# Performance work log

Hardware: AMD Instinct MI355X
Metric: run time of the kernel (lower is better)

The kernel has to match this reference:

```python
import jax, jax.numpy as jnp
import numpy as np

N_NODES = 100000
N_EDGES = 3200000
NODE_DIM = 128
MRI_DIM, COG_DIM, CLIN_DIM, GEN_DIM = 256, 64, 32, 512
N_GRAPHS = 256
N_CLASSES = 3
HID = 16


def setup_inputs() -> dict:
    key = jax.random.key(0)
    ks = jax.random.split(key, 20)
    inp = {
        "x": jax.random.normal(ks[0], (N_NODES, NODE_DIM), jnp.float32),
        "edge_index": jax.random.randint(ks[1], (2, N_EDGES), 0, N_NODES, jnp.int64),
        "batch": jnp.sort(jax.random.randint(ks[2], (N_NODES,), 0, N_GRAPHS, jnp.int64)),
        "mri": jax.random.normal(ks[3], (N_GRAPHS, MRI_DIM), jnp.float32),
        "cog": jax.random.normal(ks[4], (N_GRAPHS, COG_DIM), jnp.float32),
        "clin": jax.random.normal(ks[5], (N_GRAPHS, CLIN_DIM), jnp.float32),
        "genetic": jax.random.normal(ks[6], (N_GRAPHS, GEN_DIM), jnp.float32),
        # GCNConv weight/bias
        "gcn_W": jax.random.normal(ks[7], (NODE_DIM, HID), jnp.float32) / np.sqrt(NODE_DIM),
        "gcn_b": jnp.zeros((HID,), jnp.float32),
        # modality FCs (each -> 4)
        "mri_W": jax.random.normal(ks[8], (MRI_DIM, 4), jnp.float32) / np.sqrt(MRI_DIM),
        "mri_b": jnp.zeros((4,), jnp.float32),
        "cog_W": jax.random.normal(ks[9], (COG_DIM, 4), jnp.float32) / np.sqrt(COG_DIM),
        "cog_b": jnp.zeros((4,), jnp.float32),
        "clin_W": jax.random.normal(ks[10], (CLIN_DIM, 4), jnp.float32) / np.sqrt(CLIN_DIM),
        "clin_b": jnp.zeros((4,), jnp.float32),
        "gen_W": jax.random.normal(ks[11], (GEN_DIM, 4), jnp.float32) / np.sqrt(GEN_DIM),
        "gen_b": jnp.zeros((4,), jnp.float32),
        # classifier: Linear(32,16) -> ReLU -> Dropout(eval: identity) -> Linear(16,3)
        "cls_W1": jax.random.normal(ks[12], (32, HID), jnp.float32) / np.sqrt(32.0),
        "cls_b1": jnp.zeros((HID,), jnp.float32),
        "cls_W2": jax.random.normal(ks[13], (HID, N_CLASSES), jnp.float32) / np.sqrt(HID),
        "cls_b2": jnp.zeros((N_CLASSES,), jnp.float32),
    }
    return inp


def gcn_conv(x, edge_index, W, b):
    # PyG GCNConv: add self-loops, symmetric normalization, scatter-add.
    n = x.shape[0]
    xw = x @ W  # [N, HID]
    loop = jnp.arange(n, dtype=edge_index.dtype)
    src = jnp.concatenate([edge_index[0], loop])
    dst = jnp.concatenate([edge_index[1], loop])
    deg = jax.ops.segment_sum(jnp.ones_like(dst, dtype=xw.dtype), dst, num_segments=n)
    dinv = jnp.where(deg > 0, jax.lax.rsqrt(deg), 0.0)
    norm = dinv[src] * dinv[dst]  # [E+N]
    msg = xw[src] * norm[:, None]  # gather + scale
    out = jax.ops.segment_sum(msg, dst, num_segments=n)  # scatter-add
    return out + b


def global_mean_pool(feat, batch, num_graphs):
    s = jax.ops.segment_sum(feat, batch, num_segments=num_graphs)
    cnt = jax.ops.segment_sum(jnp.ones((feat.shape[0],), feat.dtype), batch, num_segments=num_graphs)
    return s / jnp.maximum(cnt, 1.0)[:, None]


def reference(x, edge_index, batch, mri, cog, clin, genetic,
              gcn_W, gcn_b, mri_W, mri_b, cog_W, cog_b, clin_W, clin_b,
              gen_W, gen_b, cls_W1, cls_b1, cls_W2, cls_b2):
    g = jax.nn.relu(gcn_conv(x, edge_index, gcn_W, gcn_b))  # [N, 16]
    g_emb = global_mean_pool(g, batch, N_GRAPHS)            # [B, 16]
    m = jax.nn.relu(mri @ mri_W + mri_b)
    c = jax.nn.relu(cog @ cog_W + cog_b)
    cl = jax.nn.relu(clin @ clin_W + clin_b)
    ge = jax.nn.relu(genetic @ gen_W + gen_b)
    mm = jnp.concatenate([m, c, cl, ge], axis=1)            # [B, 16]
    comb = jnp.concatenate([g_emb, mm], axis=1)             # [B, 32]
    h = jax.nn.relu(comb @ cls_W1 + cls_b1)                 # dropout is identity in eval
    logits = h @ cls_W2 + cls_b2
    return jax.nn.log_softmax(logits, axis=1)
```

## Files before the change

kernel.cpp:

```cpp
#include <hip/hip_runtime.h>
#include <hip/hip_bf16.h>
#include <math.h>

#define N_NODES   100000
#define N_EDGES   3200000
#define NODE_DIM  128
#define HID       16
#define N_GRAPHS  256

#define BSHIFT    6
#define NPB       64
#define NBUCK     ((N_NODES + NPB - 1) >> BSHIFT)
#define NBLK      256
#define TOT       (NBUCK * NBLK)
#define ACCS      17
#define STAGE     4096

#define FIX16  4096.0f
#define IFIX16 (1.0f/4096.0f)
#define FIXP   131072.0f
#define IFIXP  (1.0f/131072.0f)

__device__ __forceinline__ short f2bf(float f) {
    unsigned u = __float_as_uint(f);
    unsigned r = (u + 0x7FFF + ((u >> 16) & 1)) >> 16;
    return (short)r;
}
__device__ __forceinline__ int fx(float v, float s) { return __float2int_rn(v * s); }

typedef __attribute__((ext_vector_type(8))) short bf16x8;
typedef __attribute__((ext_vector_type(4))) float f32x4;

__global__ __launch_bounds__(1024) void bucket_count(
    const int* __restrict__ dst, int* __restrict__ Mc, int E, int chunk)
{
    __shared__ int cnt[NBUCK];
    const int t = threadIdx.x, b = blockIdx.x;
    for (int k = t; k < NBUCK; k += 1024) cnt[k] = 0;
    __syncthreads();
    int e0 = b * chunk, e1 = min(E, e0 + chunk);
    if (e1 > e0) {
        const int4* d4 = (const int4*)dst;
        for (int i = (e0 >> 2) + t; i < (e1 >> 2); i += 1024) {
            int4 d = d4[i];
            atomicAdd(&cnt[d.x >> BSHIFT], 1);
            atomicAdd(&cnt[d.y >> BSHIFT], 1);
            atomicAdd(&cnt[d.z >> BSHIFT], 1);
            atomicAdd(&cnt[d.w >> BSHIFT], 1);
        }
    }
    __syncthreads();
    for (int k = t; k < NBUCK; k += 1024) Mc[b * NBUCK + k] = cnt[k];
}

__global__ __launch_bounds__(256) void transpose_M(
    const int* __restrict__ A, int* __restrict__ At)
{
    __shared__ int tile[64][65];
    const int kt = blockIdx.x * 64, bt = blockIdx.y * 64;
    const int t = threadIdx.x, tr = t >> 6, tc = t & 63;
    for (int i = tr; i < 64; i += 4) {
        int b = bt + i, k = kt + tc;
        tile[i][tc] = (k < NBUCK) ? A[b * NBUCK + k] : 0;
    }
    __syncthreads();
    for (int i = tr; i < 64; i += 4) {
        int k = kt + i, b = bt + tc;
        if (k < NBUCK) At[k * NBLK + b] = tile[tc][i];
    }
}

__global__ __launch_bounds__(256) void scan_blocksum(
    const int* __restrict__ M, int* __restrict__ bsum, int n)
{
    __shared__ int red[256];
    int t = threadIdx.x;
    int base = blockIdx.x * 2048 + t * 8;
    int s = 0;
    #pragma unroll
    for (int k = 0; k < 8; ++k) { int i = base + k; if (i < n) s += M[i]; }
    red[t] = s; __syncthreads();
    for (int o = 128; o > 0; o >>= 1) {
        if (t < o) red[t] += red[t + o];
        __syncthreads();
    }
    if (t == 0) bsum[blockIdx.x] = red[0];
}

__global__ __launch_bounds__(256) void scan_bsums(int* __restrict__ bsum, int nb)
{
    __shared__ int tmp[256];
    int t = threadIdx.x;
    int v = (t < nb) ? bsum[t] : 0;
    tmp[t] = v; __syncthreads();
    for (int o = 1; o < 256; o <<= 1) {
        int a = (t >= o) ? tmp[t - o] : 0;
        __syncthreads();
        tmp[t] += a;
        __syncthreads();
    }
    if (t < nb) bsum[t] = tmp[t] - v;
}

__global__ __launch_bounds__(256) void scan_write(
    int* __restrict__ M, const int* __restrict__ bsum, int n)
{
    __shared__ int tsum[256];
    int t = threadIdx.x;
    int base = blockIdx.x * 2048 + t * 8;
    int v[8]; int s = 0;
    #pragma unroll
    for (int k = 0; k < 8; ++k) { int i = base + k; v[k] = (i < n) ? M[i] : 0; s += v[k]; }
    tsum[t] = s; __syncthreads();
    int mine = s;
    for (int o = 1; o < 256; o <<= 1) {
        int a = (t >= o) ? tsum[t - o] : 0;
        __syncthreads();
        tsum[t] += a;
        __syncthreads();
    }
    int pre = bsum[blockIdx.x] + tsum[t] - mine;
    #pragma unroll
    for (int k = 0; k < 8; ++k) {
        int i = base + k;
        if (i < n) { M[i] = pre; pre += v[k]; }
    }
}

__global__ __launch_bounds__(1024) void bucket_scatter(
    const int* __restrict__ src, const int* __restrict__ dst,
    const int* __restrict__ srcOff, int* __restrict__ ebuf, int E, int chunk)
{
    __shared__ int cur[NBUCK];
    const int t = threadIdx.x, b = blockIdx.x;
    for (int k = t; k < NBUCK; k += 1024) cur[k] = srcOff[b * NBUCK + k];
    __syncthreads();
    int e0 = b * chunk, e1 = min(E, e0 + chunk);
    if (e1 <= e0) return;
    const int4* d4 = (const int4*)dst;
    const int4* s4 = (const int4*)src;
    for (int i = (e0 >> 2) + t; i < (e1 >> 2); i += 1024) {
        int4 d = d4[i];
        int4 s = s4[i];
        int p;
        p = atomicAdd(&cur[d.x >> BSHIFT], 1); ebuf[p] = s.x | ((d.x & (NPB-1)) << 17);
        p = atomicAdd(&cur[d.y >> BSHIFT], 1); ebuf[p] = s.y | ((d.y & (NPB-1)) << 17);
        p = atomicAdd(&cur[d.z >> BSHIFT], 1); ebuf[p] = s.z | ((d.z & (NPB-1)) << 17);
        p = atomicAdd(&cur[d.w >> BSHIFT], 1); ebuf[p] = s.w | ((d.w & (NPB-1)) << 17);
    }
}

__global__ __launch_bounds__(256) void deg_dinv(
    const int* __restrict__ srcT, const int* __restrict__ cntT,
    const int* __restrict__ ebuf, float* __restrict__ dinv, int N)
{
    __shared__ int hist[NPB];
    const int k = blockIdx.x, t = threadIdx.x;
    if (t < NPB) hist[t] = 0;
    __syncthreads();
    int s = srcT[k * NBLK + t];
    int L = cntT[k * NBLK + t];
    #pragma unroll 4
    for (int j = 0; j < L; ++j) atomicAdd(&hist[ebuf[s + j] >> 17], 1);
    __syncthreads();
    int n = (k << BSHIFT) + t;
    if (t < NPB && n < N) dinv[n] = rsqrtf((float)(hist[t] + 1));
}

__global__ __launch_bounds__(256) void xw_kernel(
    const float* __restrict__ x, const float* __restrict__ W,
    const float* __restrict__ dinv, short* __restrict__ xws16, int N)
{
    const int t = threadIdx.x;
    const int lane = t & 63;
    const int q = lane >> 4, n = lane & 15;

    bf16x8 bfrag[4];
    #pragma unroll
    for (int i = 0; i < 4; ++i)
        #pragma unroll
        for (int j = 0; j < 8; ++j)
            bfrag[i][j] = f2bf(W[(i * 32 + q * 8 + j) * HID + n]);

    const int wave_id = blockIdx.x * 4 + (t >> 6);
    const int nwaves = gridDim.x * 4;
    const float4* x4 = (const float4*)x;
    const int ntiles = N >> 4;

    for (int tile = wave_id; tile < ntiles; tile += nwaves) {
        const int node = (tile << 4) + n;
        f32x4 d = {0.f, 0.f, 0.f, 0.f};
        #pragma unroll
        for (int i = 0; i < 4; ++i) {
            float4 u0 = x4[(size_t)node * 32 + i * 8 + q * 2];
            float4 u1 = x4[(size_t)node * 32 + i * 8 + q * 2 + 1];
            bf16x8 a;
            a[0] = f2bf(u0.x); a[1] = f2bf(u0.y); a[2] = f2bf(u0.z); a[3] = f2bf(u0.w);
            a[4] = f2bf(u1.x); a[5] = f2bf(u1.y); a[6] = f2bf(u1.z); a[7] = f2bf(u1.w);
            d = __builtin_amdgcn_mfma_f32_16x16x32_bf16(a, bfrag[i], d, 0, 0, 0);
        }
        #pragma unroll
        for (int r = 0; r < 4; ++r) {
            int nd = (tile << 4) + q * 4 + r;
            float val = d[r] * dinv[nd];
            val = fminf(7.995f, fmaxf(-7.995f, val));
            xws16[(size_t)nd * HID + n] = (short)__float2int_rn(val * FIX16);
        }
    }
}

__global__ __launch_bounds__(256, 4) void gather_pool(
    const int* __restrict__ srcT, const int* __restrict__ cntT,
    const int* __restrict__ ebuf, const float* __restrict__ dinv,
    const short* __restrict__ xws16, const float* __restrict__ gcn_b,
    const int* __restrict__ batch, int* __restrict__ pool,
    int* __restrict__ cnt, int N)
{
    __shared__ int acc[NPB * ACCS];
    __shared__ int estage[STAGE];
    __shared__ int rs[NBLK];
    __shared__ int ld[NBLK];
    __shared__ int lpool[16 * HID];
    __shared__ int lcnt[16];
    const int k = blockIdx.x, t = threadIdx.x;
    const int base = k << BSHIFT;

    for (int i = t; i < NPB * ACCS; i += 256) acc[i] = 0;
    if (t < 16 * HID) lpool[t] = 0;
    if (t < 16) lcnt[t] = 0;
    rs[t] = srcT[k * NBLK + t];
    int myLen = cntT[k * NBLK + t];
    ld[t] = myLen;
    __syncthreads();
    for (int o = 1; o < 256; o <<= 1) {
        int a = (t >= o) ? ld[t - o] : 0;
        __syncthreads();
        ld[t] += a;
        __syncthreads();
    }
    const int Ek = ld[NBLK - 1];
    const int myEnd = ld[t];
    const int myStart = myEnd - myLen;
    const int sbase = rs[t] - myStart;

    const int sub = t >> 1, h = t & 1;
    const int4* xw4 = (const int4*)xws16;

    for (int lo = 0; lo < Ek; lo += STAGE) {
        int hi = min(Ek, lo + STAGE);
        int a0 = max(myStart, lo), a1 = min(myEnd, hi);
        for (int j = a0; j < a1; ++j) estage[j - lo] = ebuf[sbase + j];
        __syncthreads();
        int len = hi - lo;
        int e = sub;
        for (; e + 3 * 128 < len; e += 512) {
            int w0 = estage[e];
            int w1 = estage[e + 128];
            int w2 = estage[e + 256];
            int w3 = estage[e + 384];
            int4 v0 = xw4[(size_t)(w0 & 0x1FFFF) * 2 + h];
            int4 v1 = xw4[(size_t)(w1 & 0x1FFFF) * 2 + h];
            int4 v2 = xw4[(size_t)(w2 & 0x1FFFF) * 2 + h];
            int4 v3 = xw4[(size_t)(w3 & 0x1FFFF) * 2 + h];
            int* p;
            p = &acc[(w0 >> 17) * ACCS + h * 8];
            atomicAdd(p + 0, (v0.x << 16) >> 16); atomicAdd(p + 1, v0.x >> 16);
            atomicAdd(p + 2, (v0.y << 16) >> 16); atomicAdd(p + 3, v0.y >> 16);
            atomicAdd(p + 4, (v0.z << 16) >> 16); atomicAdd(p + 5, v0.z >> 16);
            atomicAdd(p + 6, (v0.w << 16) >> 16); atomicAdd(p + 7, v0.w >> 16);
            p = &acc[(w1 >> 17) * ACCS + h * 8];
            atomicAdd(p + 0, (v1.x << 16) >> 16); atomicAdd(p + 1, v1.x >> 16);
            atomicAdd(p + 2, (v1.y << 16) >> 16); atomicAdd(p + 3, v1.y >> 16);
            atomicAdd(p + 4, (v1.z << 16) >> 16); atomicAdd(p + 5, v1.z >> 16);
            atomicAdd(p + 6, (v1.w << 16) >> 16); atomicAdd(p + 7, v1.w >> 16);
            p = &acc[(w2 >> 17) * ACCS + h * 8];
            atomicAdd(p + 0, (v2.x << 16) >> 16); atomicAdd(p + 1, v2.x >> 16);
            atomicAdd(p + 2, (v2.y << 16) >> 16); atomicAdd(p + 3, v2.y >> 16);
            atomicAdd(p + 4, (v2.z << 16) >> 16); atomicAdd(p + 5, v2.z >> 16);
            atomicAdd(p + 6, (v2.w << 16) >> 16); atomicAdd(p + 7, v2.w >> 16);
            p = &acc[(w3 >> 17) * ACCS + h * 8];
            atomicAdd(p + 0, (v3.x << 16) >> 16); atomicAdd(p + 1, v3.x >> 16);
            atomicAdd(p + 2, (v3.y << 16) >> 16); atomicAdd(p + 3, v3.y >> 16);
            atomicAdd(p + 4, (v3.z << 16) >> 16); atomicAdd(p + 5, v3.z >> 16);
            atomicAdd(p + 6, (v3.w << 16) >> 16); atomicAdd(p + 7, v3.w >> 16);
        }
        for (; e < len; e += 128) {
            int w = estage[e];
            int4 v = xw4[(size_t)(w & 0x1FFFF) * 2 + h];
            int* p = &acc[(w >> 17) * ACCS + h * 8];
            atomicAdd(p + 0, (v.x << 16) >> 16); atomicAdd(p + 1, v.x >> 16);
            atomicAdd(p + 2, (v.y << 16) >> 16); atomicAdd(p + 3, v.y >> 16);
            atomicAdd(p + 4, (v.z << 16) >> 16); atomicAdd(p + 5, v.z >> 16);
            atomicAdd(p + 6, (v.w << 16) >> 16); atomicAdd(p + 7, v.w >> 16);
        }
        __syncthreads();
    }

    int nN = min(NPB, N - base);
    int gmin = batch[base], gmax = batch[base + nN - 1];
    int range = gmax - gmin + 1;
    bool useL = (range <= 16);
    const int sub16 = t >> 4, lane16 = t & 15;
    float bb = gcn_b[lane16];

    for (int i = sub16; i < nN; i += 16) {
        int n = base + i;
        int tot = acc[i * ACCS + lane16] + (int)xws16[(size_t)n * HID + lane16];
        float a = (float)tot * IFIX16;
        float r = fmaxf(fmaf(dinv[n], a, bb), 0.f);
        int g = batch[n];
        int ri = fx(r, FIXP);
        if (useL) {
            atomicAdd(&lpool[(g - gmin) * HID + lane16], ri);
            if (lane16 == 0) atomicAdd(&lcnt[g - gmin], 1);
        } else {
            atomicAdd(&pool[g * HID + lane16], ri);
            if (lane16 == 0) atomicAdd(&cnt[g], 1);
        }
    }
    __syncthreads();

    if (useL) {
        for (int i = t; i < range * HID; i += 256) {
            int v = lpool[i];
            if (v != 0) atomicAdd(&pool[gmin * HID + i], v);
        }
        for (int i = t; i < range; i += 256) {
            int c = lcnt[i];
            if (c != 0) atomicAdd(&cnt[gmin + i], c);
        }
    }
}

__global__ __launch_bounds__(64) void head_kernel(
    const int* __restrict__ pool, const int* __restrict__ cnt,
    const float* __restrict__ mri,  const float* __restrict__ cog,
    const float* __restrict__ clin, const float* __restrict__ gen,
    const float* __restrict__ mriW, const float* __restrict__ mrib,
    const float* __restrict__ cogW, const float* __restrict__ cogb,
    const float* __restrict__ clinW, const float* __restrict__ clinb,
    const float* __restrict__ genW, const float* __restrict__ genb,
    const float* __restrict__ W1, const float* __restrict__ b1,
    const float* __restrict__ W2, const float* __restrict__ b2,
    float* __restrict__ out)
{
    const int g = blockIdx.x;
    const int lane = threadIdx.x;
    __shared__ float comb[32];
    __shared__ float h[HID];

    if (lane < HID) {
        float c = fmaxf((float)cnt[g], 1.f);
        comb[lane] = ((float)pool[g * HID + lane] * IFIXP) / c;
    }

    struct Mod { const float* in; const float* W; const float* b; int K; int off; };
    Mod mods[4] = {
        { mri  + (size_t)g * 256, mriW,  mrib,  256, 16 },
        { cog  + (size_t)g * 64,  cogW,  cogb,  64,  20 },
        { clin + (size_t)g * 32,  clinW, clinb, 32,  24 },
        { gen  + (size_t)g * 512, genW,  genb,  512, 28 },
    };
    for (int m = 0; m < 4; ++m) {
        float p0 = 0.f, p1 = 0.f, p2 = 0.f, p3 = 0.f;
        const float* in = mods[m].in;
        const float* Wm = mods[m].W;
        for (int kk = lane; kk < mods[m].K; kk += 64) {
            float xv = in[kk];
            p0 += xv * Wm[kk * 4 + 0];
            p1 += xv * Wm[kk * 4 + 1];
            p2 += xv * Wm[kk * 4 + 2];
            p3 += xv * Wm[kk * 4 + 3];
        }
        #pragma unroll
        for (int o = 32; o > 0; o >>= 1) {
            p0 += __shfl_down(p0, o);
            p1 += __shfl_down(p1, o);
            p2 += __shfl_down(p2, o);
            p3 += __shfl_down(p3, o);
        }
        if (lane == 0) {
            const float* bm = mods[m].b;
            int o = mods[m].off;
            comb[o + 0] = fmaxf(p0 + bm[0], 0.f);
            comb[o + 1] = fmaxf(p1 + bm[1], 0.f);
            comb[o + 2] = fmaxf(p2 + bm[2], 0.f);
            comb[o + 3] = fmaxf(p3 + bm[3], 0.f);
        }
    }
    __syncthreads();

    if (lane < HID) {
        float a = b1[lane];
        #pragma unroll
        for (int kk = 0; kk < 32; ++kk) a += comb[kk] * W1[kk * HID + lane];
        h[lane] = fmaxf(a, 0.f);
    }
    __syncthreads();

    if (lane == 0) {
        float l0 = b2[0], l1 = b2[1], l2 = b2[2];
        #pragma unroll
        for (int kk = 0; kk < HID; ++kk) {
            float hv = h[kk];
            l0 += hv * W2[kk * 3 + 0];
            l1 += hv * W2[kk * 3 + 1];
            l2 += hv * W2[kk * 3 + 2];
        }
        float mx = fmaxf(l0, fmaxf(l1, l2));
        float lse = mx + logf(expf(l0 - mx) + expf(l1 - mx) + expf(l2 - mx));
        out[g * 3 + 0] = l0 - lse;
        out[g * 3 + 1] = l1 - lse;
        out[g * 3 + 2] = l2 - lse;
    }
}

extern "C" void kernel_launch(void* const* d_in, const int* in_sizes, int n_in,
                              void* d_out, int out_size, void* d_ws, size_t ws_size,
                              hipStream_t stream)
{
    const float* x     = (const float*)d_in[0];
    const int*   eidx  = (const int*)d_in[1];
    const int*   batch = (const int*)d_in[2];
    const float* mri   = (const float*)d_in[3];
    const float* cog   = (const float*)d_in[4];
    const float* clin  = (const float*)d_in[5];
    const float* gen   = (const float*)d_in[6];
    const float* gcn_W = (const float*)d_in[7];
    const float* gcn_b = (const float*)d_in[8];
    const float* mriW  = (const float*)d_in[9];
    const float* mrib  = (const float*)d_in[10];
    const float* cogW  = (const float*)d_in[11];
    const float* cogb  = (const float*)d_in[12];
    const float* clinW = (const float*)d_in[13];
    const float* clinb = (const float*)d_in[14];
    const float* genW  = (const float*)d_in[15];
    const float* genb  = (const float*)d_in[16];
    const float* W1    = (const float*)d_in[17];
    const float* b1    = (const float*)d_in[18];
    const float* W2    = (const float*)d_in[19];
    const float* b2    = (const float*)d_in[20];
    float* out = (float*)d_out;

    const int N = in_sizes[0] / NODE_DIM;
    const int E = in_sizes[1] / 2;
    const int* src = eidx;
    const int* dst = eidx + E;

    float* ws    = (float*)d_ws;
    short* xws16 = (short*)ws;
    float* dinv  = ws + 800000;
    int*   pool  = (int*)(ws + 900000);
    int*   cnt   = (int*)(ws + 904096);
    int*   Mc    = (int*)(ws + 905000);
    int*   cntT  = (int*)(ws + 1306000);
    int*   srcT  = (int*)(ws + 1707000);
    int*   bsum  = (int*)(ws + 2108000);
    int*   ebuf  = (int*)(ws + 2109000);

    const int chunkE = (E + NBLK - 1) / NBLK;
    const int scanNB = (TOT + 2047) / 2048;
    const dim3 tgrid((NBUCK + 63) / 64, NBLK / 64);

    hipMemsetAsync(pool, 0, (N_GRAPHS * HID + N_GRAPHS) * sizeof(int), stream);

    bucket_count<<<NBLK, 1024, 0, stream>>>(dst, Mc, E, chunkE);
    transpose_M<<<tgrid, 256, 0, stream>>>(Mc, cntT);
    scan_blocksum<<<scanNB, 256, 0, stream>>>(Mc, bsum, TOT);
    scan_bsums<<<1, 256, 0, stream>>>(bsum, scanNB);
    scan_write<<<scanNB, 256, 0, stream>>>(Mc, bsum, TOT);
    transpose_M<<<tgrid, 256, 0, stream>>>(Mc, srcT);
    bucket_scatter<<<NBLK, 1024, 0, stream>>>(src, dst, Mc, ebuf, E, chunkE);
    deg_dinv<<<NBUCK, 256, 0, stream>>>(srcT, cntT, ebuf, dinv, N);
    xw_kernel<<<512, 256, 0, stream>>>(x, gcn_W, dinv, xws16, N);
    gather_pool<<<NBUCK, 256, 0, stream>>>(srcT, cntT, ebuf, dinv, xws16,
                                           gcn_b, batch, pool, cnt, N);
    head_kernel<<<N_GRAPHS, 64, 0, stream>>>(
        pool, cnt, mri, cog, clin, gen,
        mriW, mrib, cogW, cogb, clinW, clinb, genW, genb,
        W1, b1, W2, b2, out);
}
```

Measured before the change: 254.2 us.

## Fuse scan stages and degree/xw kernels, use wave-shuffle scan in gather

Merges the block-sum scan into the write kernel so each block rescans the small block-sum array itself, removing one launch. Fuses the degree histogram and the x@W MFMA projection into one per-bucket kernel that keeps dinv in shared memory, removing another launch and a global dinv reread. In gather_pool, replaces the shared-memory Hillis-Steele prefix scan with a wave shuffle scan and raises the launch_bounds occupancy hint from 4 to 7. The fused kernel maps one 16-node tile per wave with no grid-stride loop, which changes how the xw work is spread across the GPU.

After: 248.2 us. 2.3% less time.

```diff
diff --git a/kernel.cpp b/kernel.cpp
--- a/kernel.cpp
+++ b/kernel.cpp
@@ -87,26 +87,22 @@
     if (t == 0) bsum[blockIdx.x] = red[0];
 }
 
-__global__ __launch_bounds__(256) void scan_bsums(int* __restrict__ bsum, int nb)
+__global__ __launch_bounds__(256) void scan_write2(
+    int* __restrict__ M, const int* __restrict__ bsum, int n, int nb)
 {
     __shared__ int tmp[256];
+    __shared__ int tsum[256];
     int t = threadIdx.x;
-    int v = (t < nb) ? bsum[t] : 0;
-    tmp[t] = v; __syncthreads();
+    tmp[t] = (t < nb) ? bsum[t] : 0;
+    __syncthreads();
     for (int o = 1; o < 256; o <<= 1) {
         int a = (t >= o) ? tmp[t - o] : 0;
         __syncthreads();
         tmp[t] += a;
         __syncthreads();
     }
-    if (t < nb) bsum[t] = tmp[t] - v;
-}
-
-__global__ __launch_bounds__(256) void scan_write(
-    int* __restrict__ M, const int* __restrict__ bsum, int n)
-{
-    __shared__ int tsum[256];
-    int t = threadIdx.x;
+    const int pre0 = (blockIdx.x > 0) ? tmp[blockIdx.x - 1] : 0;
+
     int base = blockIdx.x * 2048 + t * 8;
     int v[8]; int s = 0;
     #pragma unroll
@@ -119,7 +115,7 @@
         tsum[t] += a;
         __syncthreads();
     }
-    int pre = bsum[blockIdx.x] + tsum[t] - mine;
+    int pre = pre0 + tsum[t] - mine;
     #pragma unroll
     for (int k = 0; k < 8; ++k) {
         int i = base + k;
@@ -150,30 +146,37 @@
     }
 }
 
-__global__ __launch_bounds__(256) void deg_dinv(
+__global__ __launch_bounds__(256) void degxw_kernel(
     const int* __restrict__ srcT, const int* __restrict__ cntT,
-    const int* __restrict__ ebuf, float* __restrict__ dinv, int N)
+    const int* __restrict__ ebuf, const float* __restrict__ x,
+    const float* __restrict__ W, float* __restrict__ dinv,
+    short* __restrict__ xws16, int N)
 {
     __shared__ int hist[NPB];
+    __shared__ float dloc[NPB];
     const int k = blockIdx.x, t = threadIdx.x;
+    const int base = k << BSHIFT;
+
     if (t < NPB) hist[t] = 0;
     __syncthreads();
-    int s = srcT[k * NBLK + t];
-    int L = cntT[k * NBLK + t];
-    #pragma unroll 4
-    for (int j = 0; j < L; ++j) atomicAdd(&hist[ebuf[s + j] >> 17], 1);
-    __syncthreads();
-    int n = (k << BSHIFT) + t;
-    if (t < NPB && n < N) dinv[n] = rsqrtf((float)(hist[t] + 1));
-}
-
-__global__ __launch_bounds__(256) void xw_kernel(
-    const float* __restrict__ x, const float* __restrict__ W,
-    const float* __restrict__ dinv, short* __restrict__ xws16, int N)
-{
-    const int t = threadIdx.x;
+    {
+        int s = srcT[k * NBLK + t];
+        int L = cntT[k * NBLK + t];
+        #pragma unroll 4
+        for (int j = 0; j < L; ++j) atomicAdd(&hist[ebuf[s + j] >> 17], 1);
+    }
+    __syncthreads();
+    if (t < NPB) {
+        float dv = rsqrtf((float)(hist[t] + 1));
+        dloc[t] = dv;
+        if (base + t < N) dinv[base + t] = dv;
+    }
+    __syncthreads();
+
     const int lane = t & 63;
     const int q = lane >> 4, n = lane & 15;
+    const int tile_base = base + (t >> 6) * 16;
+    if (tile_base >= N) return;
 
     bf16x8 bfrag[4];
     #pragma unroll
@@ -182,34 +185,33 @@
         for (int j = 0; j < 8; ++j)
             bfrag[i][j] = f2bf(W[(i * 32 + q * 8 + j) * HID + n]);
 
-    const int wave_id = blockIdx.x * 4 + (t >> 6);
-    const int nwaves = gridDim.x * 4;
     const float4* x4 = (const float4*)x;
-    const int ntiles = N >> 4;
-
-    for (int tile = wave_id; tile < ntiles; tile += nwaves) {
-        const int node = (tile << 4) + n;
-        f32x4 d = {0.f, 0.f, 0.f, 0.f};
-        #pragma unroll
-        for (int i = 0; i < 4; ++i) {
-            float4 u0 = x4[(size_t)node * 32 + i * 8 + q * 2];
-            float4 u1 = x4[(size_t)node * 32 + i * 8 + q * 2 + 1];
-            bf16x8 a;
-            a[0] = f2bf(u0.x); a[1] = f2bf(u0.y); a[2] = f2bf(u0.z); a[3] = f2bf(u0.w);
-            a[4] = f2bf(u1.x); a[5] = f2bf(u1.y); a[6] = f2bf(u1.z); a[7] = f2bf(u1.w);
-            d = __builtin_amdgcn_mfma_f32_16x16x32_bf16(a, bfrag[i], d, 0, 0, 0);
-        }
-        #pragma unroll
-        for (int r = 0; r < 4; ++r) {
-            int nd = (tile << 4) + q * 4 + r;
-            float val = d[r] * dinv[nd];
+    const int node = tile_base + n;
+    f32x4 d = {0.f, 0.f, 0.f, 0.f};
+    #pragma unroll
+    for (int i = 0; i < 4; ++i) {
+        float4 u0 = make_float4(0.f, 0.f, 0.f, 0.f), u1 = u0;
+        if (node < N) {
+            u0 = x4[(size_t)node * 32 + i * 8 + q * 2];
+            u1 = x4[(size_t)node * 32 + i * 8 + q * 2 + 1];
+        }
+        bf16x8 a;
+        a[0] = f2bf(u0.x); a[1] = f2bf(u0.y); a[2] = f2bf(u0.z); a[3] = f2bf(u0.w);
+        a[4] = f2bf(u1.x); a[5] = f2bf(u1.y); a[6] = f2bf(u1.z); a[7] = f2bf(u1.w);
+        d = __builtin_amdgcn_mfma_f32_16x16x32_bf16(a, bfrag[i], d, 0, 0, 0);
+    }
+    #pragma unroll
+    for (int r = 0; r < 4; ++r) {
+        int nd = tile_base + q * 4 + r;
+        if (nd < N) {
+            float val = d[r] * dloc[nd - base];
             val = fminf(7.995f, fmaxf(-7.995f, val));
             xws16[(size_t)nd * HID + n] = (short)__float2int_rn(val * FIX16);
         }
     }
 }
 
-__global__ __launch_bounds__(256, 4) void gather_pool(
+__global__ __launch_bounds__(256, 7) void gather_pool(
     const int* __restrict__ srcT, const int* __restrict__ cntT,
     const int* __restrict__ ebuf, const float* __restrict__ dinv,
     const short* __restrict__ xws16, const float* __restrict__ gcn_b,
@@ -218,30 +220,34 @@
 {
     __shared__ int acc[NPB * ACCS];
     __shared__ int estage[STAGE];
-    __shared__ int rs[NBLK];
-    __shared__ int ld[NBLK];
+    __shared__ int wsum[4];
     __shared__ int lpool[16 * HID];
     __shared__ int lcnt[16];
     const int k = blockIdx.x, t = threadIdx.x;
     const int base = k << BSHIFT;
+    const int wave = t >> 6, lane = t & 63;
 
     for (int i = t; i < NPB * ACCS; i += 256) acc[i] = 0;
     if (t < 16 * HID) lpool[t] = 0;
     if (t < 16) lcnt[t] = 0;
-    rs[t] = srcT[k * NBLK + t];
-    int myLen = cntT[k * NBLK + t];
-    ld[t] = myLen;
-    __syncthreads();
-    for (int o = 1; o < 256; o <<= 1) {
-        int a = (t >= o) ? ld[t - o] : 0;
-        __syncthreads();
-        ld[t] += a;
-        __syncthreads();
-    }
-    const int Ek = ld[NBLK - 1];
-    const int myEnd = ld[t];
+
+    const int myOff = srcT[k * NBLK + t];
+    const int myLen = cntT[k * NBLK + t];
+    int v = myLen;
+    #pragma unroll
+    for (int o = 1; o < 64; o <<= 1) {
+        int u = __shfl_up(v, o);
+        if (lane >= o) v += u;
+    }
+    if (lane == 63) wsum[wave] = v;
+    __syncthreads();
+    int woff = 0;
+    #pragma unroll
+    for (int w = 0; w < 4; ++w) woff += (w < wave) ? wsum[w] : 0;
+    const int Ek = wsum[0] + wsum[1] + wsum[2] + wsum[3];
+    const int myEnd = woff + v;
     const int myStart = myEnd - myLen;
-    const int sbase = rs[t] - myStart;
+    const int sbase = myOff - myStart;
 
     const int sub = t >> 1, h = t & 1;
     const int4* xw4 = (const int4*)xws16;
@@ -286,12 +292,12 @@
         }
         for (; e < len; e += 128) {
             int w = estage[e];
-            int4 v = xw4[(size_t)(w & 0x1FFFF) * 2 + h];
+            int4 vv = xw4[(size_t)(w & 0x1FFFF) * 2 + h];
             int* p = &acc[(w >> 17) * ACCS + h * 8];
-            atomicAdd(p + 0, (v.x << 16) >> 16); atomicAdd(p + 1, v.x >> 16);
-            atomicAdd(p + 2, (v.y << 16) >> 16); atomicAdd(p + 3, v.y >> 16);
-            atomicAdd(p + 4, (v.z << 16) >> 16); atomicAdd(p + 5, v.z >> 16);
-            atomicAdd(p + 6, (v.w << 16) >> 16); atomicAdd(p + 7, v.w >> 16);
+            atomicAdd(p + 0, (vv.x << 16) >> 16); atomicAdd(p + 1, vv.x >> 16);
+            atomicAdd(p + 2, (vv.y << 16) >> 16); atomicAdd(p + 3, vv.y >> 16);
+            atomicAdd(p + 4, (vv.z << 16) >> 16); atomicAdd(p + 5, vv.z >> 16);
+            atomicAdd(p + 6, (vv.w << 16) >> 16); atomicAdd(p + 7, vv.w >> 16);
         }
         __syncthreads();
     }
@@ -322,8 +328,8 @@
 
     if (useL) {
         for (int i = t; i < range * HID; i += 256) {
-            int v = lpool[i];
-            if (v != 0) atomicAdd(&pool[gmin * HID + i], v);
+            int vv = lpool[i];
+            if (vv != 0) atomicAdd(&pool[gmin * HID + i], vv);
         }
         for (int i = t; i < range; i += 256) {
             int c = lcnt[i];
@@ -467,12 +473,11 @@
     bucket_count<<<NBLK, 1024, 0, stream>>>(dst, Mc, E, chunkE);
     transpose_M<<<tgrid, 256, 0, stream>>>(Mc, cntT);
     scan_blocksum<<<scanNB, 256, 0, stream>>>(Mc, bsum, TOT);
-    scan_bsums<<<1, 256, 0, stream>>>(bsum, scanNB);
-    scan_write<<<scanNB, 256, 0, stream>>>(Mc, bsum, TOT);
+    scan_write2<<<scanNB, 256, 0, stream>>>(Mc, bsum, TOT, scanNB);
     transpose_M<<<tgrid, 256, 0, stream>>>(Mc, srcT);
     bucket_scatter<<<NBLK, 1024, 0, stream>>>(src, dst, Mc, ebuf, E, chunkE);
-    deg_dinv<<<NBUCK, 256, 0, stream>>>(srcT, cntT, ebuf, dinv, N);
-    xw_kernel<<<512, 256, 0, stream>>>(x, gcn_W, dinv, xws16, N);
+    degxw_kernel<<<NBUCK, 256, 0, stream>>>(srcT, cntT, ebuf, x, gcn_W,
+                                            dinv, xws16, N);
     gather_pool<<<NBUCK, 256, 0, stream>>>(srcT, cntT, ebuf, dinv, xws16,
                                            gcn_b, batch, pool, cnt, N);
     head_kernel<<<N_GRAPHS, 64, 0, stream>>>(
```
